# Optimization experiments

Measured on AMD Instinct MI355X. Metric: run time of the kernel, lower is better.

Reference implementation:

```python
import jax, jax.numpy as jnp
import numpy as np

B, N, F_IN, F_OUT = 8, 2048, 128, 128
ALPHA = 0.1  # leaky-relu negative slope
NEG = -9e15


def setup_inputs() -> dict:
    key = jax.random.key(0)
    k1, k2, k3, k4, k5, k6 = jax.random.split(key, 6)
    s = 1.0 / np.sqrt(F_OUT)
    return {
        "x1": jax.random.normal(k1, (B, N, F_IN), dtype=jnp.float32),
        "x2": jax.random.normal(k2, (B, N, F_IN), dtype=jnp.float32),
        "cross_weight": jax.random.uniform(k3, (F_IN, F_OUT), minval=-s, maxval=s, dtype=jnp.float32),
        "friend_weight": jax.random.uniform(k4, (F_IN, F_OUT), minval=-s, maxval=s, dtype=jnp.float32),
        "self_weight": jax.random.uniform(k5, (F_IN, F_OUT), minval=-s, maxval=s, dtype=jnp.float32),
        "att_weight": jax.random.uniform(k6, (2 * F_OUT, 1), minval=-1.0, maxval=1.0, dtype=jnp.float32),
    }


def _one_set(xq, x_others, cross_weight, friend_weight, self_weight, att_weight):
    # GAT-style additive attention for one set against cross-set + friend supports.
    fo = cross_weight.shape[1]
    a_q, a_k = att_weight[:fo], att_weight[fo:]  # split additive-attention vector
    cross = jnp.concatenate([xo @ cross_weight for xo in x_others], axis=1)  # [B, M, F]
    friend = xq @ friend_weight                                              # [B, Nq, F]
    h = jnp.concatenate([cross, friend], axis=1)                             # [B, Nk, F]
    s_q = (friend @ a_q)[..., 0]  # [B, Nq]
    s_k = (h @ a_k)[..., 0]       # [B, Nk]
    e = jax.nn.leaky_relu(s_q[:, :, None] + s_k[:, None, :], negative_slope=ALPHA)  # [B, Nq, Nk]
    nq, m = xq.shape[1], cross.shape[1]
    # mask: all cross-set keys allowed; friend keys masked on the diagonal (no self-edge)
    mask = jnp.concatenate([jnp.ones((nq, m), dtype=e.dtype),
                            1.0 - jnp.eye(nq, dtype=e.dtype)], axis=1)
    att = jax.nn.softmax(jnp.where(mask > 0, e, NEG), axis=-1)  # [B, Nq, Nk]
    out = jnp.einsum('bqk,bkf->bqf', att, h)                    # [B, Nq, F]
    return out + xq @ self_weight


def reference(x1, x2, cross_weight, friend_weight, self_weight, att_weight):
    out1 = _one_set(x1, [x2], cross_weight, friend_weight, self_weight, att_weight)
    out2 = _one_set(x2, [x1], cross_weight, friend_weight, self_weight, att_weight)
    return (out1, out2)
```

## Files before the change

### kernel.cpp

```cpp
#include <hip/hip_runtime.h>
#include <hip/hip_bf16.h>
#include <stdint.h>

typedef __attribute__((ext_vector_type(8))) short short8;
typedef __attribute__((ext_vector_type(16))) float f32x16;

#define NB 8
#define NN 2048
#define NF 128
#define NK 4096
#define L2E 1.4426950408889634f

#define OFF_HT   0u
#define OFF_WCT  16777216u
#define OFF_WFT  16809984u
#define OFF_WST  16842752u
#define OFF_U1   16875520u
#define OFF_U2   16876032u
#define OFF_U3   16876544u
#define OFF_SQ   16877056u
#define OFF_SK   17008128u

__device__ __forceinline__ short f2bf(float f){
  __bf16 h = (__bf16)f;
  return __builtin_bit_cast(short, h);
}
__device__ __forceinline__ short8 pack8(float4 a, float4 b){
  short8 r;
  r[0]=f2bf(a.x); r[1]=f2bf(a.y); r[2]=f2bf(a.z); r[3]=f2bf(a.w);
  r[4]=f2bf(b.x); r[5]=f2bf(b.y); r[6]=f2bf(b.z); r[7]=f2bf(b.w);
  return r;
}

typedef const __attribute__((address_space(1))) unsigned int* gas_t;
typedef __attribute__((address_space(3))) unsigned int* las_t;
__device__ __forceinline__ void gload_lds16(const void* g, void* l){
  __builtin_amdgcn_global_load_lds((gas_t)g, (las_t)l, 16, 0, 0);
}

__global__ __launch_bounds__(256) void k_prep(const float* __restrict__ Wc,
                                              const float* __restrict__ Wf,
                                              const float* __restrict__ Ws,
                                              const float* __restrict__ att,
                                              char* __restrict__ ws){
  int bidx = blockIdx.x, tid = threadIdx.x;
  if (bidx < 12){
    __shared__ float tile[32][129];
    int m = bidx >> 2, tno = bidx & 3;
    const float* W = (m == 0) ? Wc : ((m == 1) ? Wf : Ws);
    short* WT = (short*)(ws + ((m == 0) ? OFF_WCT : ((m == 1) ? OFF_WFT : OFF_WST)));
    int r0 = tno*32;
    #pragma unroll
    for (int i = 0; i < 16; i++){
      int e = tid + i*256;
      tile[e >> 7][e & 127] = W[(r0 + (e >> 7))*NF + (e & 127)];
    }
    __syncthreads();
    #pragma unroll
    for (int i = 0; i < 16; i++){
      int o = tid + i*256;
      int col = o >> 5, rr = o & 31;
      WT[col*NF + r0 + rr] = f2bf(tile[rr][col]);
    }
  } else {
    int wid = tid >> 6, lane = tid & 63;
    float aq0 = att[lane],      aq1 = att[64 + lane];
    float ak0 = att[NF + lane], ak1 = att[NF + 64 + lane];
    float* u1 = (float*)(ws + OFF_U1);
    float* u2 = (float*)(ws + OFF_U2);
    float* u3 = (float*)(ws + OFF_U3);
    for (int j = 0; j < 32; j++){
      int r = wid*32 + j;
      float wf0 = Wf[r*NF + lane], wf1 = Wf[r*NF + 64 + lane];
      float wc0 = Wc[r*NF + lane], wc1 = Wc[r*NF + 64 + lane];
      float s1 = wf0*aq0 + wf1*aq1;
      float s2 = wc0*ak0 + wc1*ak1;
      float s3 = wf0*ak0 + wf1*ak1;
      #pragma unroll
      for (int d = 1; d < 64; d <<= 1){
        s1 += __shfl_xor(s1, d); s2 += __shfl_xor(s2, d); s3 += __shfl_xor(s3, d);
      }
      if (lane == 0){ u1[r] = s1; u2[r] = s2; u3[r] = s3; }
    }
  }
}

__global__ __launch_bounds__(256) void k_build(const float* __restrict__ x1,
                                               const float* __restrict__ x2,
                                               char* __restrict__ ws){
  int bid = blockIdx.x;
  int xid  = bid >> 7;
  int b    = (bid >> 4) & 7;
  int tile = bid & 15;
  int tid = threadIdx.x, wid = tid >> 6, lane = tid & 63;
  int l31 = lane & 31, khalf = lane >> 5;
  int r0 = tile*128 + wid*32;
  int row = r0 + l31;

  const float* x = xid ? x2 : x1;
  const float* u1 = (const float*)(ws + OFF_U1);
  const float* u2 = (const float*)(ws + OFF_U2);
  const float* u3 = (const float*)(ws + OFF_U3);
  const float* xrow = x + (size_t)(b*NN + row)*NF;

  short8 aF[8];
  float p1=0.f, p2=0.f, p3=0.f;
  #pragma unroll
  for (int ks = 0; ks < 8; ks++){
    int k0 = ks*16 + khalf*8;
    float4 xa = *(const float4*)(xrow + k0);
    float4 xb = *(const float4*)(xrow + k0 + 4);
    float4 a1 = *(const float4*)(u1 + k0), b1 = *(const float4*)(u1 + k0 + 4);
    float4 a2 = *(const float4*)(u2 + k0), b2 = *(const float4*)(u2 + k0 + 4);
    float4 a3 = *(const float4*)(u3 + k0), b3 = *(const float4*)(u3 + k0 + 4);
    p1 += xa.x*a1.x + xa.y*a1.y + xa.z*a1.z + xa.w*a1.w
        + xb.x*b1.x + xb.y*b1.y + xb.z*b1.z + xb.w*b1.w;
    p2 += xa.x*a2.x + xa.y*a2.y + xa.z*a2.z + xa.w*a2.w
        + xb.x*b2.x + xb.y*b2.y + xb.z*b2.z + xb.w*b2.w;
    p3 += xa.x*a3.x + xa.y*a3.y + xa.z*a3.z + xa.w*a3.w
        + xb.x*b3.x + xb.y*b3.y + xb.z*b3.z + xb.w*b3.w;
    aF[ks] = pack8(xa, xb);
  }
  p1 += __shfl_xor(p1, 32);
  p2 += __shfl_xor(p2, 32);
  p3 += __shfl_xor(p3, 32);
  if (lane < 32){
    float* sq = (float*)(ws + OFF_SQ);
    float* sk = (float*)(ws + OFF_SK);
    sq[(xid*NB + b)*NN + row] = p1*L2E;
    sk[(xid*NB + b)*NK + NN + row] = p3*L2E;
    sk[((1 - xid)*NB + b)*NK + row] = p2*L2E;
  }

  short* hT = (short*)(ws + OFF_HT);
  #pragma unroll
  for (int g = 0; g < 2; g++){
    const short* W = g ? (const short*)(ws + OFF_WFT) : (const short*)(ws + OFF_WCT);
    int dset = g ? xid : (1 - xid);
    int kb2  = (g ? NN : 0) + r0;
    f32x16 acc[4] = {};
    #pragma unroll
    for (int ks = 0; ks < 8; ks++){
      #pragma unroll
      for (int cb = 0; cb < 4; cb++){
        short8 bF = *(const short8*)(W + (cb*32 + l31)*NF + ks*16 + khalf*8);
        acc[cb] = __builtin_amdgcn_mfma_f32_32x32x16_bf16(aF[ks], bF, acc[cb], 0, 0, 0);
      }
    }
    short* hbase = hT + (size_t)(dset*NB + b)*NF*NK;
    #pragma unroll
    for (int cb = 0; cb < 4; cb++){
      short* hc = hbase + (size_t)(cb*32 + l31)*NK;
      #pragma unroll
      for (int g4 = 0; g4 < 4; g4++){
        int kr = kb2 + g4*8 + khalf*4;
        uint2 v;
        v.x = (unsigned)(unsigned short)f2bf(acc[cb][4*g4+0]) |
              ((unsigned)(unsigned short)f2bf(acc[cb][4*g4+1]) << 16);
        v.y = (unsigned)(unsigned short)f2bf(acc[cb][4*g4+2]) |
              ((unsigned)(unsigned short)f2bf(acc[cb][4*g4+3]) << 16);
        *(uint2*)(hc + kr) = v;
      }
    }
  }
}

__global__ __launch_bounds__(512, 2) void k_attn(const float* __restrict__ x1,
                                              const float* __restrict__ x2,
                                              const char* __restrict__ ws,
                                              float* __restrict__ out){
  __shared__ float skb[NK];
  __shared__ __align__(16) char stg[8*16384];
  __shared__ float wmax[8];

  int hw = blockIdx.x;
  int bid = (hw & 7)*32 + (hw >> 3);
  int set = bid >> 7, b = (bid >> 4) & 7, qt = bid & 15;
  int tid = threadIdx.x, wid = tid >> 6, lane = tid & 63;
  int grp = wid >> 1, rw = wid & 1;
  int l31 = lane & 31, khalf = lane >> 5;

  const short* hT  = (const short*)(ws + OFF_HT) + (size_t)(set*NB + b)*NF*NK;
  const float* skg = (const float*)(ws + OFF_SK) + (set*NB + b)*NK;
  const float* sqg = (const float*)(ws + OFF_SQ) + (set*NB + b)*NN;
  const short* WsT = (const short*)(ws + OFF_WST);

  auto stage = [&](int it, int bufi){
    char* dst = stg + (grp*2 + bufi)*16384;
    int ch = grp*16 + it;
    #pragma unroll
    for (int i = 0; i < 8; i++){
      int u = (rw*8 + i)*64 + lane;
      int col = u >> 3, k16 = u & 7;
      int srcc = k16 ^ (col & 7);
      gload_lds16((const void*)(hT + col*NK + ch*64 + srcc*8),
                  (void*)(dst + (rw*8 + i)*1024));
    }
  };

  stage(0, 0);
  float mx = -3.0e38f;
  #pragma unroll
  for (int i = 0; i < 2; i++){
    int idx = i*2048 + tid*4;
    float4 v = *(const float4*)(skg + idx);
    *(float4*)(skb + idx) = v;
    mx = fmaxf(mx, fmaxf(fmaxf(v.x, v.y), fmaxf(v.z, v.w)));
  }
  #pragma unroll
  for (int d = 1; d < 64; d <<= 1) mx = fmaxf(mx, __shfl_xor(mx, d));
  if (lane == 0) wmax[wid] = mx;
  asm volatile("s_waitcnt lgkmcnt(0)" ::: "memory");
  asm volatile("s_barrier" ::: "memory");

  float skmax = wmax[0];
  #pragma unroll
  for (int i = 1; i < 8; i++) skmax = fmaxf(skmax, wmax[i]);

  int q0w = qt*128 + rw*64;
  float sqm[2], c9[2]; int kdiag[2];
  #pragma unroll
  for (int rb = 0; rb < 2; rb++){
    int row = q0w + rb*32 + l31;
    float sqv = sqg[row];
    float t0 = sqv + skmax;
    float moff = fmaxf(t0, 0.1f*t0);
    sqm[rb] = sqv - moff;
    c9[rb]  = -0.9f*moff;
    kdiag[rb] = NN + row;
  }
  int chd = (NN + q0w) >> 6;

  f32x16 acc[2][4] = {};
  float zacc[2] = {0.f, 0.f};

  for (int it = 0; it < 16; ++it){
    if (it < 15){
      stage(it + 1, (it + 1) & 1);
      asm volatile("s_waitcnt vmcnt(8)" ::: "memory");
    } else {
      asm volatile("s_waitcnt vmcnt(0)" ::: "memory");
    }
    asm volatile("s_barrier" ::: "memory");

    int ch = grp*16 + it;
    const char* buf = stg + (grp*2 + (it & 1))*16384;
    #pragma unroll
    for (int ks = 0; ks < 4; ks++){
      const float* skp = skb + ch*64 + ks*16 + khalf*8;
      float sv[8];
      #pragma unroll
      for (int j = 0; j < 8; j++) sv[j] = skp[j];
      short8 aw[2];
      #pragma unroll
      for (int rb = 0; rb < 2; rb++){
        float wv[8];
        #pragma unroll
        for (int j = 0; j < 8; j++){
          float p = sv[j] + sqm[rb];
          float qn = __builtin_fmaf(0.1f, p, c9[rb]);
          wv[j] = __builtin_amdgcn_exp2f(fmaxf(p, qn));
        }
        if (ch == chd){
          int kg0 = ch*64 + ks*16 + khalf*8;
          #pragma unroll
          for (int j = 0; j < 8; j++) wv[j] = (kg0 + j == kdiag[rb]) ? 0.f : wv[j];
        }
        #pragma unroll
        for (int j = 0; j < 8; j++) zacc[rb] += wv[j];
        #pragma unroll
        for (int j = 0; j < 8; j++) aw[rb][j] = f2bf(wv[j]);
      }
      #pragma unroll
      for (int cb = 0; cb < 4; cb++){
        int col = cb*32 + l31;
        int slot = (ks*2 + khalf) ^ (col & 7);
        short8 bF = *(const short8*)(buf + col*128 + slot*16);
        acc[0][cb] = __builtin_amdgcn_mfma_f32_32x32x16_bf16(aw[0], bF, acc[0][cb], 0, 0, 0);
        acc[1][cb] = __builtin_amdgcn_mfma_f32_32x32x16_bf16(aw[1], bF, acc[1][cb], 0, 0, 0);
      }
    }
    asm volatile("s_barrier" ::: "memory");
  }

  float* cbuf1 = (float*)stg;
  float* cbuf2 = (float*)(stg + 65536);
  float* zarr  = skb;
  if (grp == 1 || grp == 3){
    float* dst = (grp == 1) ? cbuf1 : cbuf2;
    #pragma unroll
    for (int rb = 0; rb < 2; rb++){
      #pragma unroll
      for (int cb = 0; cb < 4; cb++)
        #pragma unroll
        for (int r = 0; r < 16; r++)
          dst[(((rw*2 + rb)*4 + cb)*16 + r)*64 + lane] = acc[rb][cb][r];
      zarr[(wid*2 + rb)*64 + lane] = zacc[rb];
    }
  }
  __syncthreads();
  if (grp == 0 || grp == 2){
    const float* src = (grp == 0) ? cbuf1 : cbuf2;
    int swid = (grp == 0) ? (2 + rw) : (6 + rw);
    #pragma unroll
    for (int rb = 0; rb < 2; rb++){
      #pragma unroll
      for (int cb = 0; cb < 4; cb++)
        #pragma unroll
        for (int r = 0; r < 16; r++)
          acc[rb][cb][r] += src[(((rw*2 + rb)*4 + cb)*16 + r)*64 + lane];
      zacc[rb] += zarr[(swid*2 + rb)*64 + lane];
    }
  }
  __syncthreads();
  if (grp == 2){
    #pragma unroll
    for (int rb = 0; rb < 2; rb++){
      #pragma unroll
      for (int cb = 0; cb < 4; cb++)
        #pragma unroll
        for (int r = 0; r < 16; r++)
          cbuf1[(((rw*2 + rb)*4 + cb)*16 + r)*64 + lane] = acc[rb][cb][r];
      zarr[((4 + rw)*2 + rb)*64 + lane] = zacc[rb];
    }
  }
  __syncthreads();
  if (grp == 0){
    #pragma unroll
    for (int rb = 0; rb < 2; rb++){
      #pragma unroll
      for (int cb = 0; cb < 4; cb++)
        #pragma unroll
        for (int r = 0; r < 16; r++)
          acc[rb][cb][r] += cbuf1[(((rw*2 + rb)*4 + cb)*16 + r)*64 + lane];
      zacc[rb] += zarr[((4 + rw)*2 + rb)*64 + lane];
    }
    const float* x = set ? x2 : x1;
    float* op = out + (size_t)(set*NB + b)*NN*NF;
    #pragma unroll
    for (int rb = 0; rb < 2; rb++){
      float zr = zacc[rb] + __shfl_xor(zacc[rb], 32);
      float rz = 1.0f / zr;
      float rzv[16];
      #pragma unroll
      for (int r = 0; r < 16; r++){
        int rowc = (r & 3) + 8*(r >> 2) + 4*khalf;
        rzv[r] = __shfl(rz, rowc);
      }
      #pragma unroll
      for (int cb = 0; cb < 4; cb++)
        #pragma unroll
        for (int r = 0; r < 16; r++) acc[rb][cb][r] *= rzv[r];

      const float* xrow = x + (size_t)(b*NN + q0w + rb*32 + l31)*NF;
      #pragma unroll
      for (int ks8 = 0; ks8 < 8; ks8++){
        int k0 = ks8*16 + khalf*8;
        float4 xa = *(const float4*)(xrow + k0);
        float4 xb = *(const float4*)(xrow + k0 + 4);
        short8 aF = pack8(xa, xb);
        #pragma unroll
        for (int cb = 0; cb < 4; cb++){
          short8 bF = *(const short8*)(WsT + (cb*32 + l31)*NF + k0);
          acc[rb][cb] = __builtin_amdgcn_mfma_f32_32x32x16_bf16(aF, bF, acc[rb][cb], 0, 0, 0);
        }
      }
      #pragma unroll
      for (int cb = 0; cb < 4; cb++)
        #pragma unroll
        for (int r = 0; r < 16; r++){
          int rowc = (r & 3) + 8*(r >> 2) + 4*khalf;
          op[(size_t)(q0w + rb*32 + rowc)*NF + cb*32 + l31] = acc[rb][cb][r];
        }
    }
  }
}

extern "C" void kernel_launch(void* const* d_in, const int* in_sizes, int n_in,
                              void* d_out, int out_size, void* d_ws, size_t ws_size,
                              hipStream_t stream){
  const float* x1  = (const float*)d_in[0];
  const float* x2  = (const float*)d_in[1];
  const float* Wc  = (const float*)d_in[2];
  const float* Wf  = (const float*)d_in[3];
  const float* Ws  = (const float*)d_in[4];
  const float* att = (const float*)d_in[5];
  char* ws = (char*)d_ws;
  float* out = (float*)d_out;

  k_prep<<<dim3(13),  dim3(256), 0, stream>>>(Wc, Wf, Ws, att, ws);
  k_build<<<dim3(256), dim3(256), 0, stream>>>(x1, x2, ws);
  k_attn<<<dim3(256), dim3(512), 0, stream>>>(x1, x2, ws, out);
}
```

Baseline: 171.9 us.

## Restructure attention kernel to 64-row tiles with 4 waves and no block barriers in loop

The attention kernel moves from 256 blocks of 512 threads (128 query rows, 8 waves in 4 key groups) to 512 blocks of 256 threads (64 query rows, 4 waves each owning a quarter of the keys). Each wave now stages its own LDS tile per iteration with a synchronous wait instead of a double-buffered pipeline guarded by block barriers. Key scores are read straight from global memory rather than from an LDS copy. The cross-wave reduction is rewritten as one all-to-all exchange, after which every wave finishes one 32-column slice, so the epilogue is shared instead of handled by a single group. The aim is more blocks, less barrier traffic and a parallel epilogue, at the cost of no load/compute overlap within a wave and twice the per-block score-max and staging overhead.

```diff
diff --git a/kernel.cpp b/kernel.cpp
--- a/kernel.cpp
+++ b/kernel.cpp
@@ -165,19 +165,17 @@
   }
 }
 
-__global__ __launch_bounds__(512, 2) void k_attn(const float* __restrict__ x1,
-                                              const float* __restrict__ x2,
-                                              const char* __restrict__ ws,
-                                              float* __restrict__ out){
-  __shared__ float skb[NK];
-  __shared__ __align__(16) char stg[8*16384];
-  __shared__ float wmax[8];
+__global__ __launch_bounds__(256, 2) void k_attn(const float* __restrict__ x1,
+                                                 const float* __restrict__ x2,
+                                                 const char* __restrict__ ws,
+                                                 float* __restrict__ out){
+  __shared__ __align__(16) char stg[4][16384];
+  __shared__ float zl[4][2][64];
 
   int hw = blockIdx.x;
-  int bid = (hw & 7)*32 + (hw >> 3);
-  int set = bid >> 7, b = (bid >> 4) & 7, qt = bid & 15;
-  int tid = threadIdx.x, wid = tid >> 6, lane = tid & 63;
-  int grp = wid >> 1, rw = wid & 1;
+  int bid = (hw & 7)*64 + (hw >> 3);
+  int set = bid >> 8, b = (bid >> 5) & 7, qt = bid & 31;
+  int tid = threadIdx.x, g = tid >> 6, lane = tid & 63;
   int l31 = lane & 31, khalf = lane >> 5;
 
   const short* hT  = (const short*)(ws + OFF_HT) + (size_t)(set*NB + b)*NF*NK;
@@ -185,39 +183,25 @@
   const float* sqg = (const float*)(ws + OFF_SQ) + (set*NB + b)*NN;
   const short* WsT = (const short*)(ws + OFF_WST);
 
-  auto stage = [&](int it, int bufi){
-    char* dst = stg + (grp*2 + bufi)*16384;
-    int ch = grp*16 + it;
-    #pragma unroll
-    for (int i = 0; i < 8; i++){
-      int u = (rw*8 + i)*64 + lane;
-      int col = u >> 3, k16 = u & 7;
-      int srcc = k16 ^ (col & 7);
-      gload_lds16((const void*)(hT + col*NK + ch*64 + srcc*8),
-                  (void*)(dst + (rw*8 + i)*1024));
-    }
-  };
-
-  stage(0, 0);
+  int soff[16];
+  #pragma unroll
+  for (int i = 0; i < 16; i++){
+    int u = i*64 + lane;
+    int col = u >> 3, k16 = u & 7;
+    soff[i] = col*NK + (k16 ^ (col & 7))*8;
+  }
+
   float mx = -3.0e38f;
   #pragma unroll
-  for (int i = 0; i < 2; i++){
-    int idx = i*2048 + tid*4;
-    float4 v = *(const float4*)(skg + idx);
-    *(float4*)(skb + idx) = v;
+  for (int i = 0; i < 16; i++){
+    float4 v = *(const float4*)(skg + i*256 + lane*4);
     mx = fmaxf(mx, fmaxf(fmaxf(v.x, v.y), fmaxf(v.z, v.w)));
   }
   #pragma unroll
   for (int d = 1; d < 64; d <<= 1) mx = fmaxf(mx, __shfl_xor(mx, d));
-  if (lane == 0) wmax[wid] = mx;
-  asm volatile("s_waitcnt lgkmcnt(0)" ::: "memory");
-  asm volatile("s_barrier" ::: "memory");
-
-  float skmax = wmax[0];
-  #pragma unroll
-  for (int i = 1; i < 8; i++) skmax = fmaxf(skmax, wmax[i]);
-
-  int q0w = qt*128 + rw*64;
+  float skmax = mx;
+
+  int q0w = qt*64;
   float sqm[2], c9[2]; int kdiag[2];
   #pragma unroll
   for (int rb = 0; rb < 2; rb++){
@@ -233,24 +217,27 @@
 
   f32x16 acc[2][4] = {};
   float zacc[2] = {0.f, 0.f};
+  char* buf = stg[g];
+  int rdswz = l31 & 7;
 
   for (int it = 0; it < 16; ++it){
-    if (it < 15){
-      stage(it + 1, (it + 1) & 1);
-      asm volatile("s_waitcnt vmcnt(8)" ::: "memory");
-    } else {
-      asm volatile("s_waitcnt vmcnt(0)" ::: "memory");
-    }
-    asm volatile("s_barrier" ::: "memory");
-
-    int ch = grp*16 + it;
-    const char* buf = stg + (grp*2 + (it & 1))*16384;
+    int ch = g*16 + it;
+    asm volatile("s_waitcnt lgkmcnt(0)" ::: "memory");
+    __builtin_amdgcn_sched_barrier(0);
+    const short* hsrc = hT + ch*64;
+    #pragma unroll
+    for (int i = 0; i < 16; i++)
+      gload_lds16((const void*)(hsrc + soff[i]), (void*)(buf + i*1024));
+    asm volatile("s_waitcnt vmcnt(0)" ::: "memory");
+    __builtin_amdgcn_sched_barrier(0);
+
     #pragma unroll
     for (int ks = 0; ks < 4; ks++){
-      const float* skp = skb + ch*64 + ks*16 + khalf*8;
-      float sv[8];
-      #pragma unroll
-      for (int j = 0; j < 8; j++) sv[j] = skp[j];
+      const float* skp = skg + ch*64 + ks*16 + khalf*8;
+      float4 sa = *(const float4*)skp;
+      float4 sb = *(const float4*)(skp + 4);
+      float sv[8] = {sa.x, sa.y, sa.z, sa.w, sb.x, sb.y, sb.z, sb.w};
+      int kg0 = ch*64 + ks*16 + khalf*8;
       short8 aw[2];
       #pragma unroll
       for (int rb = 0; rb < 2; rb++){
@@ -262,7 +249,6 @@
           wv[j] = __builtin_amdgcn_exp2f(fmaxf(p, qn));
         }
         if (ch == chd){
-          int kg0 = ch*64 + ks*16 + khalf*8;
           #pragma unroll
           for (int j = 0; j < 8; j++) wv[j] = (kg0 + j == kdiag[rb]) ? 0.f : wv[j];
         }
@@ -271,107 +257,70 @@
         #pragma unroll
         for (int j = 0; j < 8; j++) aw[rb][j] = f2bf(wv[j]);
       }
+      int slot = (ks*2 + khalf) ^ rdswz;
       #pragma unroll
       for (int cb = 0; cb < 4; cb++){
-        int col = cb*32 + l31;
-        int slot = (ks*2 + khalf) ^ (col & 7);
-        short8 bF = *(const short8*)(buf + col*128 + slot*16);
+        short8 bF = *(const short8*)(buf + (cb*32 + l31)*128 + slot*16);
         acc[0][cb] = __builtin_amdgcn_mfma_f32_32x32x16_bf16(aw[0], bF, acc[0][cb], 0, 0, 0);
         acc[1][cb] = __builtin_amdgcn_mfma_f32_32x32x16_bf16(aw[1], bF, acc[1][cb], 0, 0, 0);
       }
     }
-    asm volatile("s_barrier" ::: "memory");
-  }
-
-  float* cbuf1 = (float*)stg;
-  float* cbuf2 = (float*)(stg + 65536);
-  float* zarr  = skb;
-  if (grp == 1 || grp == 3){
-    float* dst = (grp == 1) ? cbuf1 : cbuf2;
-    #pragma unroll
-    for (int rb = 0; rb < 2; rb++){
-      #pragma unroll
-      for (int cb = 0; cb < 4; cb++)
-        #pragma unroll
-        for (int r = 0; r < 16; r++)
-          dst[(((rw*2 + rb)*4 + cb)*16 + r)*64 + lane] = acc[rb][cb][r];
-      zarr[(wid*2 + rb)*64 + lane] = zacc[rb];
-    }
-  }
-  __syncthreads();
-  if (grp == 0 || grp == 2){
-    const float* src = (grp == 0) ? cbuf1 : cbuf2;
-    int swid = (grp == 0) ? (2 + rw) : (6 + rw);
-    #pragma unroll
-    for (int rb = 0; rb < 2; rb++){
-      #pragma unroll
-      for (int cb = 0; cb < 4; cb++)
-        #pragma unroll
-        for (int r = 0; r < 16; r++)
-          acc[rb][cb][r] += src[(((rw*2 + rb)*4 + cb)*16 + r)*64 + lane];
-      zacc[rb] += zarr[(swid*2 + rb)*64 + lane];
-    }
-  }
-  __syncthreads();
-  if (grp == 2){
-    #pragma unroll
-    for (int rb = 0; rb < 2; rb++){
-      #pragma unroll
-      for (int cb = 0; cb < 4; cb++)
-        #pragma unroll
-        for (int r = 0; r < 16; r++)
-          cbuf1[(((rw*2 + rb)*4 + cb)*16 + r)*64 + lane] = acc[rb][cb][r];
-      zarr[((4 + rw)*2 + rb)*64 + lane] = zacc[rb];
-    }
-  }
-  __syncthreads();
-  if (grp == 0){
-    #pragma unroll
-    for (int rb = 0; rb < 2; rb++){
-      #pragma unroll
-      for (int cb = 0; cb < 4; cb++)
-        #pragma unroll
-        for (int r = 0; r < 16; r++)
-          acc[rb][cb][r] += cbuf1[(((rw*2 + rb)*4 + cb)*16 + r)*64 + lane];
-      zacc[rb] += zarr[((4 + rw)*2 + rb)*64 + lane];
-    }
-    const float* x = set ? x2 : x1;
-    float* op = out + (size_t)(set*NB + b)*NN*NF;
-    #pragma unroll
-    for (int rb = 0; rb < 2; rb++){
-      float zr = zacc[rb] + __shfl_xor(zacc[rb], 32);
-      float rz = 1.0f / zr;
-      float rzv[16];
-      #pragma unroll
-      for (int r = 0; r < 16; r++){
-        int rowc = (r & 3) + 8*(r >> 2) + 4*khalf;
-        rzv[r] = __shfl(rz, rowc);
-      }
-      #pragma unroll
-      for (int cb = 0; cb < 4; cb++)
-        #pragma unroll
-        for (int r = 0; r < 16; r++) acc[rb][cb][r] *= rzv[r];
-
-      const float* xrow = x + (size_t)(b*NN + q0w + rb*32 + l31)*NF;
-      #pragma unroll
-      for (int ks8 = 0; ks8 < 8; ks8++){
-        int k0 = ks8*16 + khalf*8;
-        float4 xa = *(const float4*)(xrow + k0);
-        float4 xb = *(const float4*)(xrow + k0 + 4);
-        short8 aF = pack8(xa, xb);
-        #pragma unroll
-        for (int cb = 0; cb < 4; cb++){
-          short8 bF = *(const short8*)(WsT + (cb*32 + l31)*NF + k0);
-          acc[rb][cb] = __builtin_amdgcn_mfma_f32_32x32x16_bf16(aF, bF, acc[rb][cb], 0, 0, 0);
-        }
-      }
-      #pragma unroll
-      for (int cb = 0; cb < 4; cb++)
-        #pragma unroll
-        for (int r = 0; r < 16; r++){
-          int rowc = (r & 3) + 8*(r >> 2) + 4*khalf;
-          op[(size_t)(q0w + rb*32 + rowc)*NF + cb*32 + l31] = acc[rb][cb][r];
-        }
+  }
+
+  zl[g][0][lane] = zacc[0];
+  zl[g][1][lane] = zacc[1];
+  float* comb = (float*)stg;
+  f32x16 accF[2];
+  #pragma unroll
+  for (int rb = 0; rb < 2; rb++){
+    __syncthreads();
+    #pragma unroll
+    for (int c = 0; c < 4; c++)
+      #pragma unroll
+      for (int r = 0; r < 16; r++)
+        comb[((c*4 + g)*16 + r)*64 + lane] = acc[rb][c][r];
+    __syncthreads();
+    #pragma unroll
+    for (int r = 0; r < 16; r++){
+      float s = 0.f;
+      #pragma unroll
+      for (int src = 0; src < 4; src++)
+        s += comb[((g*4 + src)*16 + r)*64 + lane];
+      accF[rb][r] = s;
+    }
+  }
+
+  const float* x = set ? x2 : x1;
+  float* op = out + (size_t)(set*NB + b)*NN*NF;
+  #pragma unroll
+  for (int rb = 0; rb < 2; rb++){
+    float zfull = 0.f;
+    #pragma unroll
+    for (int w = 0; w < 4; w++) zfull += zl[w][rb][l31] + zl[w][rb][l31 + 32];
+    float rz = 1.0f / zfull;
+    float rzv[16];
+    #pragma unroll
+    for (int r = 0; r < 16; r++){
+      int rowc = (r & 3) + 8*(r >> 2) + 4*khalf;
+      rzv[r] = __shfl(rz, rowc);
+    }
+    #pragma unroll
+    for (int r = 0; r < 16; r++) accF[rb][r] *= rzv[r];
+
+    const float* xrow = x + (size_t)(b*NN + q0w + rb*32 + l31)*NF;
+    #pragma unroll
+    for (int ks8 = 0; ks8 < 8; ks8++){
+      int k0 = ks8*16 + khalf*8;
+      float4 xa = *(const float4*)(xrow + k0);
+      float4 xb = *(const float4*)(xrow + k0 + 4);
+      short8 aF = pack8(xa, xb);
+      short8 bF = *(const short8*)(WsT + (g*32 + l31)*NF + k0);
+      accF[rb] = __builtin_amdgcn_mfma_f32_32x32x16_bf16(aF, bF, accF[rb], 0, 0, 0);
+    }
+    #pragma unroll
+    for (int r = 0; r < 16; r++){
+      int rowc = (r & 3) + 8*(r >> 2) + 4*khalf;
+      op[(size_t)(q0w + rb*32 + rowc)*NF + g*32 + l31] = accF[rb][r];
     }
   }
 }
@@ -390,5 +339,5 @@
 
   k_prep<<<dim3(13),  dim3(256), 0, stream>>>(Wc, Wf, Ws, att, ws);
   k_build<<<dim3(256), dim3(256), 0, stream>>>(x1, x2, ws);
-  k_attn<<<dim3(256), dim3(512), 0, stream>>>(x1, x2, ws, out);
-}
+  k_attn<<<dim3(512), dim3(256), 0, stream>>>(x1, x2, ws, out);
+}
```

Result: slower. 185.9 us (+8.2%).
